# Performance work log

Measured on AMD Instinct MI355X. Metric: run time of the kernel, lower is better.

## Reference

```python
import jax, jax.numpy as jnp
import numpy as np

N, E = 50000, 800000
H, C = 4, 32          # heads, per-head channels
IN_DIM = 128
NEG_SLOPE = 0.2


def gat_conv(x, edge_index, W, a_src, a_dst, b):
    """PyG-style GATConv: Wx, per-edge leaky-relu logits, dst-segment softmax,
    scatter-weighted aggregation, concat heads, add bias. Self-loops added."""
    n = x.shape[0]
    loops = jnp.arange(n, dtype=edge_index.dtype)
    src = jnp.concatenate([edge_index[0], loops])
    dst = jnp.concatenate([edge_index[1], loops])
    xw = (x @ W).reshape(n, H, C)                      # [N,H,C]
    alpha_src = jnp.sum(xw * a_src, axis=-1)           # [N,H]
    alpha_dst = jnp.sum(xw * a_dst, axis=-1)           # [N,H]
    e = jax.nn.leaky_relu(alpha_src[src] + alpha_dst[dst], NEG_SLOPE)  # [E+N,H]
    m = jax.ops.segment_max(e, dst, num_segments=n)    # stable softmax per dst
    e = jnp.exp(e - m[dst])
    denom = jax.ops.segment_sum(e, dst, num_segments=n)
    alpha = e / denom[dst]                             # [E+N,H]
    out = jax.ops.segment_sum(alpha[:, :, None] * xw[src], dst, num_segments=n)
    return out.reshape(n, H * C) + b


def setup_inputs() -> dict:
    key = jax.random.key(0)
    ks = jax.random.split(key, 12)
    HC = H * C
    x = jax.random.normal(ks[0], (N, IN_DIM), dtype=jnp.float32)
    edge_index = jax.random.randint(ks[1], (2, E), 0, N, dtype=jnp.int32)
    s0 = 1.0 / np.sqrt(IN_DIM)
    s1 = 1.0 / np.sqrt(HC)
    return {
        "x": x,
        "edge_index": edge_index,
        "W0": jax.random.normal(ks[2], (IN_DIM, HC), dtype=jnp.float32) * s0,
        "a_src0": jax.random.normal(ks[3], (H, C), dtype=jnp.float32) * s1,
        "a_dst0": jax.random.normal(ks[4], (H, C), dtype=jnp.float32) * s1,
        "b0": jnp.zeros((HC,), dtype=jnp.float32),
        "W1": jax.random.normal(ks[5], (HC, HC), dtype=jnp.float32) * s1,
        "a_src1": jax.random.normal(ks[6], (H, C), dtype=jnp.float32) * s1,
        "a_dst1": jax.random.normal(ks[7], (H, C), dtype=jnp.float32) * s1,
        "b1": jnp.zeros((HC,), dtype=jnp.float32),
        "Wr": jax.random.normal(ks[8], (HC, 1), dtype=jnp.float32) * s1,
        "br": jnp.zeros((1,), dtype=jnp.float32),
    }


def reference(x, edge_index, W0, a_src0, a_dst0, b0, W1, a_src1, a_dst1, b1, Wr, br):
    h = jax.nn.elu(gat_conv(x, edge_index, W0, a_src0, a_dst0, b0))
    # F.dropout(training=False) -> identity (eval mode)
    h = jax.nn.elu(gat_conv(h, edge_index, W1, a_src1, a_dst1, b1))
    return h @ Wr + br
```

## Files before the change

kernel.cpp:

```cpp
#include <hip/hip_runtime.h>
#include <hip/hip_bf16.h>
#include <hip/hip_fp16.h>

#define DEV __device__ __forceinline__

DEV float lrelu(float x) { return x > 0.f ? x : 0.2f * x; }
DEV float elu(float x)   { return x > 0.f ? x : __expf(x) - 1.f; }

#define CAP 64

__global__ void scatter_fused(const int* __restrict__ ei, int* __restrict__ deg,
                              int* __restrict__ col2, int E) {
    int e = blockIdx.x * 256 + threadIdx.x;
    if (e < E) {
        int s = ei[e], d = ei[E + e];
        int pos = atomicAdd(&deg[d], 1);
        if (pos < CAP) col2[d * CAP + pos] = s;
    }
}

__global__ __launch_bounds__(256, 5)
void gemm_alpha_v6(const float* __restrict__ X, const float* __restrict__ W,
                   const float* __restrict__ a_src, const float* __restrict__ a_dst,
                   __half2* __restrict__ xw2, float* __restrict__ asrc,
                   float* __restrict__ adst, int n) {
    __shared__ float Xs[32][68];
    __shared__ float Ws[32][132];
    int t = threadIdx.x;
    int n0 = blockIdx.x * 64;
    int rg = t >> 4;
    int cg = t & 15;
    int q0 = cg * 8 + ((cg >= 8) ? 4 : 0);

    float acc[4][8];
#pragma unroll
    for (int r = 0; r < 4; ++r)
#pragma unroll
        for (int c = 0; c < 8; ++c) acc[r][c] = 0.f;

    float4 px[2], pw[4];
    auto load_x = [&](int k0, float4* p) {
#pragma unroll
        for (int it = 0; it < 2; ++it) {
            int idx = t + it * 256;
            int row = idx >> 3, kq = idx & 7;
            int gr = n0 + row;
            p[it] = (gr < n) ? *(const float4*)&X[(size_t)gr * 128 + k0 + kq * 4]
                             : make_float4(0.f, 0.f, 0.f, 0.f);
        }
    };
    auto load_w = [&](int k0, float4* p) {
#pragma unroll
        for (int it = 0; it < 4; ++it) {
            int idx = t + it * 256;
            int k = idx >> 5, cq = idx & 31;
            p[it] = *(const float4*)&W[(size_t)(k0 + k) * 128 + cq * 4];
        }
    };
    auto store_lds = [&](const float4* pX, const float4* pW) {
#pragma unroll
        for (int it = 0; it < 2; ++it) {
            int idx = t + it * 256;
            int row = idx >> 3, kq = idx & 7;
            Xs[kq * 4 + 0][row] = pX[it].x;
            Xs[kq * 4 + 1][row] = pX[it].y;
            Xs[kq * 4 + 2][row] = pX[it].z;
            Xs[kq * 4 + 3][row] = pX[it].w;
        }
#pragma unroll
        for (int it = 0; it < 4; ++it) {
            int idx = t + it * 256;
            int k = idx >> 5, cq = idx & 31;
            *(float4*)&Ws[k][cq * 4 + ((cq >= 16) ? 4 : 0)] = pW[it];
        }
    };

    load_x(0, px);
    load_w(0, pw);
    for (int c4 = 0; c4 < 4; ++c4) {
        store_lds(px, pw);
        __syncthreads();
        if (c4 < 3) { load_x((c4 + 1) * 32, px); load_w((c4 + 1) * 32, pw); }
#pragma unroll 4
        for (int k = 0; k < 32; ++k) {
            float4 xv = *(const float4*)&Xs[k][rg * 4];
            float4 w0 = *(const float4*)&Ws[k][q0];
            float4 w1 = *(const float4*)&Ws[k][q0 + 4];
            float xr[4] = {xv.x, xv.y, xv.z, xv.w};
            float wr[8] = {w0.x, w0.y, w0.z, w0.w, w1.x, w1.y, w1.z, w1.w};
#pragma unroll
            for (int r = 0; r < 4; ++r)
#pragma unroll
                for (int c = 0; c < 8; ++c)
                    acc[r][c] = fmaf(xr[r], wr[c], acc[r][c]);
        }
        __syncthreads();
    }

    int c0 = cg * 8;
    int h = cg >> 2;
    float as8[8], ad8[8];
#pragma unroll
    for (int c = 0; c < 8; ++c) { as8[c] = a_src[c0 + c]; ad8[c] = a_dst[c0 + c]; }
#pragma unroll
    for (int r = 0; r < 4; ++r) {
        int gr = n0 + rg * 4 + r;
        float s_ = 0.f, d_ = 0.f;
#pragma unroll
        for (int c = 0; c < 8; ++c) {
            s_ = fmaf(acc[r][c], as8[c], s_);
            d_ = fmaf(acc[r][c], ad8[c], d_);
        }
        s_ += __shfl_xor(s_, 1); s_ += __shfl_xor(s_, 2);
        d_ += __shfl_xor(d_, 1); d_ += __shfl_xor(d_, 2);
        if (gr < n) {
            __half2* rowp = &xw2[(size_t)gr * 64 + (c0 >> 1)];
            rowp[0] = __floats2half2_rn(acc[r][0], acc[r][1]);
            rowp[1] = __floats2half2_rn(acc[r][2], acc[r][3]);
            rowp[2] = __floats2half2_rn(acc[r][4], acc[r][5]);
            rowp[3] = __floats2half2_rn(acc[r][6], acc[r][7]);
            if ((t & 3) == 0) { asrc[gr * 4 + h] = s_; adst[gr * 4 + h] = d_; }
        }
    }
}

__global__ __launch_bounds__(256, 8)
void aggregate_v7(const __half2* __restrict__ xw2, const float* __restrict__ asrc,
                  const float* __restrict__ adst, const int* __restrict__ col2,
                  const int* __restrict__ deg, const float* __restrict__ bias,
                  float* __restrict__ out128, float* __restrict__ out1,
                  const float* __restrict__ Wr, const float* __restrict__ br, int n) {
    int l = threadIdx.x & 63;
    int i = __builtin_amdgcn_readfirstlane((blockIdx.x * 256 + threadIdx.x) >> 6);
    if (i >= n) return;
    int h4 = l & 3;
    int jj = l >> 2;
    int hA = l >> 4;
    int beg = i * CAP;
    int dcount = deg[i]; if (dcount > CAP) dcount = CAP;
    int end = beg + dcount;
    float ad = adst[i * 4 + h4];
    float wsum = __expf(lrelu(asrc[i * 4 + h4] + ad));
    float wselfA = __shfl(wsum, hA);
    float2 row_i = __half22float2(xw2[(size_t)i * 64 + l]);
    float2 a0 = make_float2(wselfA * row_i.x, wselfA * row_i.y);
    float2 a1 = make_float2(0.f, 0.f);
    float2 a2 = make_float2(0.f, 0.f);
    float2 a3 = make_float2(0.f, 0.f);

    int ce = beg;
    for (; ce + 16 <= end; ce += 16) {
        int s = col2[ce + jj];
        float wv = __expf(lrelu(asrc[s * 4 + h4] + ad));
        float sv = wv;
        sv += __shfl_xor(sv, 4);
        sv += __shfl_xor(sv, 8);
        sv += __shfl_xor(sv, 16);
        sv += __shfl_xor(sv, 32);
        wsum += sv;
#pragma unroll
        for (int j = 0; j < 16; j += 4) {
            int s0 = col2[ce + j + 0];
            int s1 = col2[ce + j + 1];
            int s2 = col2[ce + j + 2];
            int s3 = col2[ce + j + 3];
            float g0 = __shfl(wv, (j + 0) * 4 + hA);
            float g1 = __shfl(wv, (j + 1) * 4 + hA);
            float g2 = __shfl(wv, (j + 2) * 4 + hA);
            float g3 = __shfl(wv, (j + 3) * 4 + hA);
            float2 v0 = __half22float2(xw2[(size_t)s0 * 64 + l]);
            float2 v1 = __half22float2(xw2[(size_t)s1 * 64 + l]);
            float2 v2 = __half22float2(xw2[(size_t)s2 * 64 + l]);
            float2 v3 = __half22float2(xw2[(size_t)s3 * 64 + l]);
            a0.x = fmaf(g0, v0.x, a0.x); a0.y = fmaf(g0, v0.y, a0.y);
            a1.x = fmaf(g1, v1.x, a1.x); a1.y = fmaf(g1, v1.y, a1.y);
            a2.x = fmaf(g2, v2.x, a2.x); a2.y = fmaf(g2, v2.y, a2.y);
            a3.x = fmaf(g3, v3.x, a3.x); a3.y = fmaf(g3, v3.y, a3.y);
        }
    }
    if (ce < end) {
        int nc = end - ce;
        float wv = 0.f;
        if (jj < nc) {
            int s = col2[ce + jj];
            wv = __expf(lrelu(asrc[s * 4 + h4] + ad));
        }
        float sv = wv;
        sv += __shfl_xor(sv, 4);
        sv += __shfl_xor(sv, 8);
        sv += __shfl_xor(sv, 16);
        sv += __shfl_xor(sv, 32);
        wsum += sv;
#pragma unroll
        for (int j = 0; j < 16; ++j) {
            if (j >= nc) break;
            int sj = col2[ce + j];
            float wg = __shfl(wv, j * 4 + hA);
            float2 v = __half22float2(xw2[(size_t)sj * 64 + l]);
            a0.x = fmaf(wg, v.x, a0.x);
            a0.y = fmaf(wg, v.y, a0.y);
        }
    }
    a0.x += (a1.x + a2.x) + a3.x;
    a0.y += (a1.y + a2.y) + a3.y;
    float wsA = __shfl(wsum, hA);
    float inv = 1.f / wsA;
    float2 bv = *(const float2*)&bias[2 * l];
    float rx = elu(a0.x * inv + bv.x);
    float ry = elu(a0.y * inv + bv.y);
    if (out1 == nullptr) {
        *(float2*)&out128[(size_t)i * 128 + 2 * l] = make_float2(rx, ry);
    } else {
        float v = rx * Wr[2 * l] + ry * Wr[2 * l + 1];
#pragma unroll
        for (int off = 32; off > 0; off >>= 1) v += __shfl_xor(v, off);
        if (l == 0) out1[i] = v + br[0];
    }
}

extern "C" void kernel_launch(void* const* d_in, const int* in_sizes, int n_in,
                              void* d_out, int out_size, void* d_ws, size_t ws_size,
                              hipStream_t stream) {
    const float* x   = (const float*)d_in[0];
    const int*   ei  = (const int*)d_in[1];
    const float* W0  = (const float*)d_in[2];
    const float* as0 = (const float*)d_in[3];
    const float* ad0 = (const float*)d_in[4];
    const float* b0  = (const float*)d_in[5];
    const float* W1  = (const float*)d_in[6];
    const float* as1 = (const float*)d_in[7];
    const float* ad1 = (const float*)d_in[8];
    const float* b1  = (const float*)d_in[9];
    const float* Wr  = (const float*)d_in[10];
    const float* br  = (const float*)d_in[11];
    float* out = (float*)d_out;

    const int N = in_sizes[0] / 128;
    const int E = in_sizes[1] / 2;

    char* w = (char*)d_ws;
    size_t off = 0;
    auto alloc = [&](size_t bytes) -> void* {
        void* p = w + off;
        off += (bytes + 255) & ~size_t(255);
        return p;
    };
    __half2* xw2  = (__half2*)alloc((size_t)N * 64 * 4);
    float* bufB   = (float*)alloc((size_t)N * 128 * 4);
    float* asrc   = (float*)alloc((size_t)N * 4 * 4);
    float* adst   = (float*)alloc((size_t)N * 4 * 4);
    int*   deg    = (int*)alloc((size_t)N * 4);
    int*   col2   = (int*)alloc((size_t)N * CAP * 4);

    hipMemsetAsync(deg, 0, (size_t)N * 4, stream);
    scatter_fused<<<(E + 255) / 256, 256, 0, stream>>>(ei, deg, col2, E);

    int gblk = (N + 63) / 64;
    int ablk = (N + 3) / 4;
    gemm_alpha_v6<<<gblk, 256, 0, stream>>>(x, W0, as0, ad0, xw2, asrc, adst, N);
    aggregate_v7<<<ablk, 256, 0, stream>>>(xw2, asrc, adst, col2, deg, b0, bufB,
                                           nullptr, nullptr, nullptr, N);
    gemm_alpha_v6<<<gblk, 256, 0, stream>>>(bufB, W1, as1, ad1, xw2, asrc, adst, N);
    aggregate_v7<<<ablk, 256, 0, stream>>>(xw2, asrc, adst, col2, deg, b1, nullptr,
                                           out, Wr, br, N);
}
```

Baseline: 307.2 us.

## Fuse edge scatter and first GEMM into one heterogeneous launch

Merges the edge-to-CSR scatter kernel and the first-layer GEMM+alpha kernel into a single launch. The first 768 blocks run a grid-stride atomic scatter while the remaining blocks compute the GEMM tiles, so the two independent stages overlap on the GPU and one launch is removed. The trade-offs are that scatter blocks now follow the GEMM's launch bounds and LDS allocation, and the scatter uses fewer blocks than before.

New measurement: 294.5 us. 4.1% less time.

```diff
diff --git a/kernel.cpp b/kernel.cpp
--- a/kernel.cpp
+++ b/kernel.cpp
@@ -9,13 +9,119 @@
 
 #define CAP 64
 
-__global__ void scatter_fused(const int* __restrict__ ei, int* __restrict__ deg,
-                              int* __restrict__ col2, int E) {
-    int e = blockIdx.x * 256 + threadIdx.x;
-    if (e < E) {
-        int s = ei[e], d = ei[E + e];
-        int pos = atomicAdd(&deg[d], 1);
-        if (pos < CAP) col2[d * CAP + pos] = s;
+__global__ __launch_bounds__(256, 5)
+void scatter_gemm0(const int* __restrict__ ei, int* __restrict__ deg,
+                   int* __restrict__ col2, int E, int sblk,
+                   const float* __restrict__ X, const float* __restrict__ W,
+                   const float* __restrict__ a_src, const float* __restrict__ a_dst,
+                   __half2* __restrict__ xw2, float* __restrict__ asrc,
+                   float* __restrict__ adst, int n) {
+    if ((int)blockIdx.x < sblk) {
+        int stride = sblk * 256;
+        for (int e = blockIdx.x * 256 + threadIdx.x; e < E; e += stride) {
+            int s = ei[e], d = ei[E + e];
+            int pos = atomicAdd(&deg[d], 1);
+            if (pos < CAP) col2[d * CAP + pos] = s;
+        }
+        return;
+    }
+    __shared__ float Xs[32][68];
+    __shared__ float Ws[32][132];
+    int t = threadIdx.x;
+    int n0 = ((int)blockIdx.x - sblk) * 64;
+    int rg = t >> 4;
+    int cg = t & 15;
+    int q0 = cg * 8 + ((cg >= 8) ? 4 : 0);
+
+    float acc[4][8];
+#pragma unroll
+    for (int r = 0; r < 4; ++r)
+#pragma unroll
+        for (int c = 0; c < 8; ++c) acc[r][c] = 0.f;
+
+    float4 px[2], pw[4];
+    auto load_x = [&](int k0, float4* p) {
+#pragma unroll
+        for (int it = 0; it < 2; ++it) {
+            int idx = t + it * 256;
+            int row = idx >> 3, kq = idx & 7;
+            int gr = n0 + row;
+            p[it] = (gr < n) ? *(const float4*)&X[(size_t)gr * 128 + k0 + kq * 4]
+                             : make_float4(0.f, 0.f, 0.f, 0.f);
+        }
+    };
+    auto load_w = [&](int k0, float4* p) {
+#pragma unroll
+        for (int it = 0; it < 4; ++it) {
+            int idx = t + it * 256;
+            int k = idx >> 5, cq = idx & 31;
+            p[it] = *(const float4*)&W[(size_t)(k0 + k) * 128 + cq * 4];
+        }
+    };
+    auto store_lds = [&](const float4* pX, const float4* pW) {
+#pragma unroll
+        for (int it = 0; it < 2; ++it) {
+            int idx = t + it * 256;
+            int row = idx >> 3, kq = idx & 7;
+            Xs[kq * 4 + 0][row] = pX[it].x;
+            Xs[kq * 4 + 1][row] = pX[it].y;
+            Xs[kq * 4 + 2][row] = pX[it].z;
+            Xs[kq * 4 + 3][row] = pX[it].w;
+        }
+#pragma unroll
+        for (int it = 0; it < 4; ++it) {
+            int idx = t + it * 256;
+            int k = idx >> 5, cq = idx & 31;
+            *(float4*)&Ws[k][cq * 4 + ((cq >= 16) ? 4 : 0)] = pW[it];
+        }
+    };
+
+    load_x(0, px);
+    load_w(0, pw);
+    for (int c4 = 0; c4 < 4; ++c4) {
+        store_lds(px, pw);
+        __syncthreads();
+        if (c4 < 3) { load_x((c4 + 1) * 32, px); load_w((c4 + 1) * 32, pw); }
+#pragma unroll 4
+        for (int k = 0; k < 32; ++k) {
+            float4 xv = *(const float4*)&Xs[k][rg * 4];
+            float4 w0 = *(const float4*)&Ws[k][q0];
+            float4 w1 = *(const float4*)&Ws[k][q0 + 4];
+            float xr[4] = {xv.x, xv.y, xv.z, xv.w};
+            float wr[8] = {w0.x, w0.y, w0.z, w0.w, w1.x, w1.y, w1.z, w1.w};
+#pragma unroll
+            for (int r = 0; r < 4; ++r)
+#pragma unroll
+                for (int c = 0; c < 8; ++c)
+                    acc[r][c] = fmaf(xr[r], wr[c], acc[r][c]);
+        }
+        __syncthreads();
+    }
+
+    int c0 = cg * 8;
+    int h = cg >> 2;
+    float as8[8], ad8[8];
+#pragma unroll
+    for (int c = 0; c < 8; ++c) { as8[c] = a_src[c0 + c]; ad8[c] = a_dst[c0 + c]; }
+#pragma unroll
+    for (int r = 0; r < 4; ++r) {
+        int gr = n0 + rg * 4 + r;
+        float s_ = 0.f, d_ = 0.f;
+#pragma unroll
+        for (int c = 0; c < 8; ++c) {
+            s_ = fmaf(acc[r][c], as8[c], s_);
+            d_ = fmaf(acc[r][c], ad8[c], d_);
+        }
+        s_ += __shfl_xor(s_, 1); s_ += __shfl_xor(s_, 2);
+        d_ += __shfl_xor(d_, 1); d_ += __shfl_xor(d_, 2);
+        if (gr < n) {
+            __half2* rowp = &xw2[(size_t)gr * 64 + (c0 >> 1)];
+            rowp[0] = __floats2half2_rn(acc[r][0], acc[r][1]);
+            rowp[1] = __floats2half2_rn(acc[r][2], acc[r][3]);
+            rowp[2] = __floats2half2_rn(acc[r][4], acc[r][5]);
+            rowp[3] = __floats2half2_rn(acc[r][6], acc[r][7]);
+            if ((t & 3) == 0) { asrc[gr * 4 + h] = s_; adst[gr * 4 + h] = d_; }
+        }
     }
 }
 
@@ -253,11 +359,12 @@
     int*   col2   = (int*)alloc((size_t)N * CAP * 4);
 
     hipMemsetAsync(deg, 0, (size_t)N * 4, stream);
-    scatter_fused<<<(E + 255) / 256, 256, 0, stream>>>(ei, deg, col2, E);
-
-    int gblk = (N + 63) / 64;
-    int ablk = (N + 3) / 4;
-    gemm_alpha_v6<<<gblk, 256, 0, stream>>>(x, W0, as0, ad0, xw2, asrc, adst, N);
+
+    const int sblk = 768;
+    const int gblk = (N + 63) / 64;
+    const int ablk = (N + 3) / 4;
+    scatter_gemm0<<<sblk + gblk, 256, 0, stream>>>(ei, deg, col2, E, sblk,
+                                                   x, W0, as0, ad0, xw2, asrc, adst, N);
     aggregate_v7<<<ablk, 256, 0, stream>>>(xw2, asrc, adst, col2, deg, b0, bufB,
                                            nullptr, nullptr, nullptr, N);
     gemm_alpha_v6<<<gblk, 256, 0, stream>>>(bufB, W1, as1, ad1, xw2, asrc, adst, N);
```
